# Optimization experiments

Measured on AMD Instinct MI355X. Metric: run time of the kernel, lower is better.

Reference implementation:

```python
import jax, jax.numpy as jnp
import numpy as np

B, S, D, H = 128, 1024, 512, 512


def setup_inputs() -> dict:
    key = jax.random.key(0)
    ks = jax.random.split(key, 8)
    return {
        "input": jax.random.normal(ks[0], (B, D), jnp.float32),
        "context": jax.random.normal(ks[1], (B, S, D), jnp.float32),
        "mask": jax.random.randint(ks[2], (B, S), 0, 2).astype(bool),
        "W_in": jax.random.normal(ks[3], (H, D), jnp.float32) * (1.0 / np.sqrt(D)),
        "b_in": jax.random.normal(ks[4], (H,), jnp.float32) * 0.01,
        "W_ctx": jax.random.normal(ks[5], (H, D), jnp.float32) * (1.0 / np.sqrt(D)),
        "b_ctx": jax.random.normal(ks[6], (H,), jnp.float32) * 0.01,
        "V": jax.random.uniform(ks[7], (H,), jnp.float32, -1.0, 1.0),
    }


def reference(input, context, mask, W_in, b_in, W_ctx, b_ctx, V):
    # inp: [B, H] -> broadcast over S (torch: unsqueeze(2).expand)
    inp = input @ W_in.T + b_in
    # 1x1 Conv1d over permuted context == per-position linear: [B, H, S]
    ctx = jnp.einsum('bsd,hd->bhs', context, W_ctx) + b_ctx[None, :, None]
    # additive (Bahdanau) score: V . tanh(inp + ctx) over H -> [B, S]
    att = jnp.einsum('h,bhs->bs', V, jnp.tanh(inp[:, :, None] + ctx))
    att = jnp.where(mask, -jnp.inf, att)
    alpha = jax.nn.softmax(att, axis=-1)  # [B, S]
    # weighted sum of projected context: [B, H]
    hidden_state = jnp.einsum('bhs,bs->bh', ctx, alpha)
    return (hidden_state, alpha)
```

## Files before the change

### kernel.cpp

```cpp
#include <hip/hip_runtime.h>
#include <math.h>

#define B_ 128
#define S_ 1024
#define D_ 512
#define H_ 512

typedef _Float16 f16x2 __attribute__((ext_vector_type(2)));
typedef _Float16 f16x4 __attribute__((ext_vector_type(4)));
typedef _Float16 f16x8 __attribute__((ext_vector_type(8)));
typedef float    f32x4 __attribute__((ext_vector_type(4)));

__global__ void zero_k(float* __restrict__ p, int n) {
    int i = blockIdx.x * 256 + threadIdx.x;
    if (i < n) p[i] = 0.f;
}

__global__ void init2_k(float* __restrict__ att, float* __restrict__ hidden,
                        const float* __restrict__ bc) {
    int i = blockIdx.x * 256 + threadIdx.x;
    if (i < B_ * S_) att[i] = 0.f;
    else if (i < B_ * S_ + B_ * H_) {
        int j = i - B_ * S_;
        hidden[j] = bc[j & (H_ - 1)];
    }
}

__global__ __launch_bounds__(256) void linear_k(const float* __restrict__ X,
                                                const float* __restrict__ W,
                                                const float* __restrict__ bias,
                                                float* __restrict__ out) {
    int idx = blockIdx.x * 256 + threadIdx.x;
    int b = idx >> 9;
    int h = idx & 511;
    const float4* x = (const float4*)(X + (size_t)b * D_);
    const float4* w = (const float4*)(W + (size_t)h * D_);
    float s = 0.f;
#pragma unroll 8
    for (int k = 0; k < D_ / 4; ++k) {
        float4 xv = x[k], wv = w[k];
        s = fmaf(xv.x, wv.x, s);
        s = fmaf(xv.y, wv.y, s);
        s = fmaf(xv.z, wv.z, s);
        s = fmaf(xv.w, wv.w, s);
    }
    out[idx] = s + bias[h];
}

__device__ inline f16x4 cvt4(float4 v) {
    f16x4 r;
    r[0] = (_Float16)v.x; r[1] = (_Float16)v.y;
    r[2] = (_Float16)v.z; r[3] = (_Float16)v.w;
    return r;
}

__device__ inline float fast_tanh(float x) {
    float e = __expf(2.f * x);
    return 1.f - 2.f / (e + 1.f);
}

template <bool WCTX>
__global__ __launch_bounds__(256) void score_mfma(const float* __restrict__ ctx,
                                                  const float* __restrict__ Wc,
                                                  const float* __restrict__ bc,
                                                  const float* __restrict__ Vv,
                                                  const float* __restrict__ inp,
                                                  float* __restrict__ att,
                                                  _Float16* __restrict__ ctxp) {
    __shared__ __align__(16) _Float16 Ah[128][40];
    __shared__ __align__(16) _Float16 Bh[128][40];
    __shared__ float red[8][128];

    const int tid = threadIdx.x;
    const int s0 = blockIdx.x * 128;
    const int h0 = blockIdx.y * 128;
    const int b  = blockIdx.z;

    const int rb  = tid >> 3;
    const int grp = tid & 7;

    const int wave = tid >> 6;
    const int lane = tid & 63;
    const int wm = wave >> 1, wn = wave & 1;
    const int l15 = lane & 15, quad = lane >> 4;

    const float* Abase = Wc  + (size_t)(h0 + rb) * D_ + grp * 4;
    const float* Bbase = ctx + ((size_t)b * S_ + s0 + rb) * D_ + grp * 4;

    f32x4 acc[4][4];
#pragma unroll
    for (int mi = 0; mi < 4; ++mi)
#pragma unroll
        for (int ni = 0; ni < 4; ++ni) acc[mi][ni] = (f32x4){0.f, 0.f, 0.f, 0.f};

    float4 ra[4], rbv[4];
#pragma unroll
    for (int i = 0; i < 4; ++i) {
        ra[i]  = *(const float4*)(Abase + (size_t)(32 * i) * D_);
        rbv[i] = *(const float4*)(Bbase + (size_t)(32 * i) * D_);
    }

    for (int k0 = 0; k0 < D_; k0 += 32) {
        __syncthreads();
#pragma unroll
        for (int i = 0; i < 4; ++i) {
            const int row = rb + 32 * i;
            *(f16x4*)&Ah[row][grp * 4] = cvt4(ra[i]);
            *(f16x4*)&Bh[row][grp * 4] = cvt4(rbv[i]);
        }
        __syncthreads();
        if (k0 + 32 < D_) {
#pragma unroll
            for (int i = 0; i < 4; ++i) {
                ra[i]  = *(const float4*)(Abase + (size_t)(32 * i) * D_ + k0 + 32);
                rbv[i] = *(const float4*)(Bbase + (size_t)(32 * i) * D_ + k0 + 32);
            }
        }
        f16x8 bhf[4];
#pragma unroll
        for (int ni = 0; ni < 4; ++ni)
            bhf[ni] = *(const f16x8*)&Bh[wn * 64 + ni * 16 + l15][quad * 8];
#pragma unroll
        for (int mi = 0; mi < 4; ++mi) {
            f16x8 ah = *(const f16x8*)&Ah[wm * 64 + mi * 16 + l15][quad * 8];
#pragma unroll
            for (int ni = 0; ni < 4; ++ni)
                acc[mi][ni] = __builtin_amdgcn_mfma_f32_16x16x32_f16(ah, bhf[ni], acc[mi][ni], 0, 0, 0);
        }
    }

    if (WCTX) {
#pragma unroll
        for (int ni = 0; ni < 4; ++ni) {
            const size_t srow = ((size_t)b * S_ + s0 + wn * 64 + ni * 16 + l15) * H_;
#pragma unroll
            for (int mi = 0; mi < 4; ++mi) {
                f16x4 v;
                v[0] = (_Float16)acc[mi][ni][0];
                v[1] = (_Float16)acc[mi][ni][1];
                v[2] = (_Float16)acc[mi][ni][2];
                v[3] = (_Float16)acc[mi][ni][3];
                *(f16x4*)(ctxp + srow + h0 + wm * 64 + mi * 16 + quad * 4) = v;
            }
        }
    }

    float p[4] = {0.f, 0.f, 0.f, 0.f};
#pragma unroll
    for (int mi = 0; mi < 4; ++mi) {
#pragma unroll
        for (int r = 0; r < 4; ++r) {
            const int h = h0 + wm * 64 + mi * 16 + quad * 4 + r;
            const float c  = inp[(size_t)b * H_ + h] + bc[h];
            const float vh = Vv[h];
#pragma unroll
            for (int ni = 0; ni < 4; ++ni)
                p[ni] = fmaf(vh, fast_tanh(c + acc[mi][ni][r]), p[ni]);
        }
    }
    const int cid = wm * 4 + quad;
#pragma unroll
    for (int ni = 0; ni < 4; ++ni)
        red[cid][wn * 64 + ni * 16 + l15] = p[ni];
    __syncthreads();
    if (tid < 128) {
        float s = 0.f;
#pragma unroll
        for (int g = 0; g < 8; ++g) s += red[g][tid];
        atomicAdd(att + (size_t)b * S_ + s0 + tid, s);
    }
}

__global__ __launch_bounds__(256) void softmax_k(const float* __restrict__ att,
                                                 const int* __restrict__ mask,
                                                 float* __restrict__ alpha) {
    const int b = blockIdx.x;
    const int t = threadIdx.x;
    __shared__ float sm[256];
    float v[4];
    float mx = -INFINITY;
#pragma unroll
    for (int i = 0; i < 4; ++i) {
        int s = t + i * 256;
        float a = att[(size_t)b * S_ + s];
        int mk = mask[(size_t)b * S_ + s];
        v[i] = mk ? -INFINITY : a;
        mx = fmaxf(mx, v[i]);
    }
    sm[t] = mx;
    __syncthreads();
    for (int off = 128; off > 0; off >>= 1) {
        if (t < off) sm[t] = fmaxf(sm[t], sm[t + off]);
        __syncthreads();
    }
    mx = sm[0];
    __syncthreads();
    float e[4];
    float sum = 0.f;
#pragma unroll
    for (int i = 0; i < 4; ++i) {
        e[i] = expf(v[i] - mx);
        sum += e[i];
    }
    sm[t] = sum;
    __syncthreads();
    for (int off = 128; off > 0; off >>= 1) {
        if (t < off) sm[t] += sm[t + off];
        __syncthreads();
    }
    float inv = 1.f / sm[0];
#pragma unroll
    for (int i = 0; i < 4; ++i) alpha[(size_t)b * S_ + t + i * 256] = e[i] * inv;
}

__global__ __launch_bounds__(256) void cbar2_k(const _Float16* __restrict__ ctxp,
                                               const float* __restrict__ alpha,
                                               float* __restrict__ hidden) {
    const int b  = blockIdx.y;
    const int s0 = blockIdx.x * 128;
    const int t  = threadIdx.x;
    const int w = t >> 6, lane = t & 63;
    __shared__ float al[128];
    __shared__ float red[3][512];
    if (t < 128) al[t] = alpha[(size_t)b * S_ + s0 + t];
    __syncthreads();
    const _Float16* base = ctxp + ((size_t)b * S_ + s0) * H_ + lane * 8;
    float acc[8] = {0.f, 0.f, 0.f, 0.f, 0.f, 0.f, 0.f, 0.f};
#pragma unroll 4
    for (int s = w; s < 128; s += 4) {
        float a = al[s];
        f16x8 v = *(const f16x8*)(base + (size_t)s * H_);
#pragma unroll
        for (int j = 0; j < 8; ++j) acc[j] = fmaf(a, (float)v[j], acc[j]);
    }
    if (w > 0) {
#pragma unroll
        for (int j = 0; j < 8; ++j) red[w - 1][lane * 8 + j] = acc[j];
    }
    __syncthreads();
    if (w == 0) {
        float* dst = hidden + (size_t)b * H_ + lane * 8;
#pragma unroll
        for (int j = 0; j < 8; ++j)
            atomicAdd(dst + j, acc[j] + red[0][lane * 8 + j] + red[1][lane * 8 + j] + red[2][lane * 8 + j]);
    }
}

__global__ __launch_bounds__(256) void cbar_k(const float* __restrict__ ctx,
                                              const float* __restrict__ alpha,
                                              float* __restrict__ cbar) {
    const int b = blockIdx.y;
    const int s0 = blockIdx.x * 128;
    const int t = threadIdx.x;
    const int c4 = t & 127;
    const int sh = t >> 7;
    __shared__ float al[128];
    __shared__ float4 red[128];
    if (t < 128) al[t] = alpha[(size_t)b * S_ + s0 + t];
    __syncthreads();
    const float4* base = (const float4*)(ctx + ((size_t)b * S_ + s0) * D_);
    float4 c = {0.f, 0.f, 0.f, 0.f};
#pragma unroll 4
    for (int s = sh; s < 128; s += 2) {
        float a = al[s];
        float4 x = base[(size_t)s * (D_ / 4) + c4];
        c.x = fmaf(a, x.x, c.x);
        c.y = fmaf(a, x.y, c.y);
        c.z = fmaf(a, x.z, c.z);
        c.w = fmaf(a, x.w, c.w);
    }
    if (sh == 1) red[c4] = c;
    __syncthreads();
    if (sh == 0) {
        float4 o = red[c4];
        float* dst = cbar + (size_t)b * D_ + c4 * 4;
        atomicAdd(dst + 0, c.x + o.x);
        atomicAdd(dst + 1, c.y + o.y);
        atomicAdd(dst + 2, c.z + o.z);
        atomicAdd(dst + 3, c.w + o.w);
    }
}

extern "C" void kernel_launch(void* const* d_in, const int* in_sizes, int n_in,
                              void* d_out, int out_size, void* d_ws, size_t ws_size,
                              hipStream_t stream) {
    const float* input = (const float*)d_in[0];
    const float* ctx   = (const float*)d_in[1];
    const int*   mask  = (const int*)d_in[2];
    const float* W_in  = (const float*)d_in[3];
    const float* b_in  = (const float*)d_in[4];
    const float* W_ctx = (const float*)d_in[5];
    const float* b_ctx = (const float*)d_in[6];
    const float* V     = (const float*)d_in[7];

    float* hidden = (float*)d_out;
    float* alpha  = (float*)d_out + B_ * H_;

    float* inp  = (float*)d_ws;
    float* att  = inp + B_ * H_;
    float* cbar = att + B_ * S_;
    _Float16* ctxp = (_Float16*)(cbar + B_ * D_);

    const size_t base_bytes = (size_t)(B_ * H_ + B_ * S_ + B_ * D_) * sizeof(float);
    const size_t ctxp_bytes = (size_t)B_ * S_ * H_ * sizeof(_Float16);
    const bool big = ws_size >= base_bytes + ctxp_bytes;

    dim3 g2(S_ / 128, H_ / 128, B_);

    if (big) {
        int ni = B_ * S_ + B_ * H_;
        init2_k<<<(ni + 255) / 256, 256, 0, stream>>>(att, hidden, b_ctx);

        linear_k<<<(B_ * H_) / 256, 256, 0, stream>>>(input, W_in, b_in, inp);

        score_mfma<true><<<g2, 256, 0, stream>>>(ctx, W_ctx, b_ctx, V, inp, att, ctxp);

        softmax_k<<<B_, 256, 0, stream>>>(att, mask, alpha);

        dim3 g4(S_ / 128, B_);
        cbar2_k<<<g4, 256, 0, stream>>>(ctxp, alpha, hidden);
    } else {
        int nz = B_ * S_ + B_ * D_;
        zero_k<<<(nz + 255) / 256, 256, 0, stream>>>(att, nz);

        linear_k<<<(B_ * H_) / 256, 256, 0, stream>>>(input, W_in, b_in, inp);

        score_mfma<false><<<g2, 256, 0, stream>>>(ctx, W_ctx, b_ctx, V, inp, att, nullptr);

        softmax_k<<<B_, 256, 0, stream>>>(att, mask, alpha);

        dim3 g4(S_ / 128, B_);
        cbar_k<<<g4, 256, 0, stream>>>(ctx, alpha, cbar);

        linear_k<<<(B_ * H_) / 256, 256, 0, stream>>>(cbar, W_ctx, b_ctx, hidden);
    }
}
```

Baseline: 567.6 us.

## Double-buffer LDS tiles with XOR swizzle and 16-byte fp16 stores in score GEMM

Replaces the single padded LDS tile and its two barriers per k-step with a ping-pong pair of unpadded buffers, so one barrier per step separates writing the next tile from computing on the current one. Each thread now loads 8 consecutive floats per row and writes a full f16x8 into LDS, at a column offset XOR-swizzled by the row to avoid bank conflicts without padding. The intent is to cut barrier stalls and LDS store instructions and to overlap global loads with MFMA work. In exchange it uses more LDS and adds swizzle index math.

```diff
diff --git a/kernel.cpp b/kernel.cpp
--- a/kernel.cpp
+++ b/kernel.cpp
@@ -6,7 +6,6 @@
 #define D_ 512
 #define H_ 512
 
-typedef _Float16 f16x2 __attribute__((ext_vector_type(2)));
 typedef _Float16 f16x4 __attribute__((ext_vector_type(4)));
 typedef _Float16 f16x8 __attribute__((ext_vector_type(8)));
 typedef float    f32x4 __attribute__((ext_vector_type(4)));
@@ -47,10 +46,12 @@
     out[idx] = s + bias[h];
 }
 
-__device__ inline f16x4 cvt4(float4 v) {
-    f16x4 r;
-    r[0] = (_Float16)v.x; r[1] = (_Float16)v.y;
-    r[2] = (_Float16)v.z; r[3] = (_Float16)v.w;
+__device__ inline f16x8 cvt8(float4 a, float4 b) {
+    f16x8 r;
+    r[0] = (_Float16)a.x; r[1] = (_Float16)a.y;
+    r[2] = (_Float16)a.z; r[3] = (_Float16)a.w;
+    r[4] = (_Float16)b.x; r[5] = (_Float16)b.y;
+    r[6] = (_Float16)b.z; r[7] = (_Float16)b.w;
     return r;
 }
 
@@ -67,8 +68,8 @@
                                                   const float* __restrict__ inp,
                                                   float* __restrict__ att,
                                                   _Float16* __restrict__ ctxp) {
-    __shared__ __align__(16) _Float16 Ah[128][40];
-    __shared__ __align__(16) _Float16 Bh[128][40];
+    __shared__ __align__(16) _Float16 Ah[2][128][32];
+    __shared__ __align__(16) _Float16 Bh[2][128][32];
     __shared__ float red[8][128];
 
     const int tid = threadIdx.x;
@@ -76,16 +77,20 @@
     const int h0 = blockIdx.y * 128;
     const int b  = blockIdx.z;
 
-    const int rb  = tid >> 3;
-    const int grp = tid & 7;
+    const int r0  = tid >> 2;
+    const int kg  = tid & 3;
+    const int swz = ((kg ^ (r0 & 3)) << 3);
 
     const int wave = tid >> 6;
     const int lane = tid & 63;
     const int wm = wave >> 1, wn = wave & 1;
     const int l15 = lane & 15, quad = lane >> 4;
-
-    const float* Abase = Wc  + (size_t)(h0 + rb) * D_ + grp * 4;
-    const float* Bbase = ctx + ((size_t)b * S_ + s0 + rb) * D_ + grp * 4;
+    const int rdsw = ((quad ^ (l15 & 3)) << 3);
+
+    const float* Arow0 = Wc  + (size_t)(h0 + r0) * D_ + kg * 8;
+    const float* Arow1 = Arow0 + (size_t)64 * D_;
+    const float* Brow0 = ctx + ((size_t)b * S_ + s0 + r0) * D_ + kg * 8;
+    const float* Brow1 = Brow0 + (size_t)64 * D_;
 
     f32x4 acc[4][4];
 #pragma unroll
@@ -93,41 +98,52 @@
 #pragma unroll
         for (int ni = 0; ni < 4; ++ni) acc[mi][ni] = (f32x4){0.f, 0.f, 0.f, 0.f};
 
-    float4 ra[4], rbv[4];
-#pragma unroll
-    for (int i = 0; i < 4; ++i) {
-        ra[i]  = *(const float4*)(Abase + (size_t)(32 * i) * D_);
-        rbv[i] = *(const float4*)(Bbase + (size_t)(32 * i) * D_);
-    }
-
-    for (int k0 = 0; k0 < D_; k0 += 32) {
+    float4 A0a, A0b, A1a, A1b, B0a, B0b, B1a, B1b;
+
+#define LOADS(step) do { const int kk_ = (step) * 32;                               \
+    A0a = *(const float4*)(Arow0 + kk_); A0b = *(const float4*)(Arow0 + kk_ + 4);   \
+    A1a = *(const float4*)(Arow1 + kk_); A1b = *(const float4*)(Arow1 + kk_ + 4);   \
+    B0a = *(const float4*)(Brow0 + kk_); B0b = *(const float4*)(Brow0 + kk_ + 4);   \
+    B1a = *(const float4*)(Brow1 + kk_); B1b = *(const float4*)(Brow1 + kk_ + 4); } while (0)
+
+#define WRITE(bf) do {                                                              \
+    *(f16x8*)&Ah[bf][r0][swz]      = cvt8(A0a, A0b);                                \
+    *(f16x8*)&Ah[bf][r0 + 64][swz] = cvt8(A1a, A1b);                                \
+    *(f16x8*)&Bh[bf][r0][swz]      = cvt8(B0a, B0b);                                \
+    *(f16x8*)&Bh[bf][r0 + 64][swz] = cvt8(B1a, B1b); } while (0)
+
+#define COMPUTE(bf) do {                                                            \
+    f16x8 bhf_[4];                                                                  \
+    _Pragma("unroll")                                                               \
+    for (int ni = 0; ni < 4; ++ni)                                                  \
+        bhf_[ni] = *(const f16x8*)&Bh[bf][wn * 64 + ni * 16 + l15][rdsw];           \
+    _Pragma("unroll")                                                               \
+    for (int mi = 0; mi < 4; ++mi) {                                                \
+        f16x8 ah_ = *(const f16x8*)&Ah[bf][wm * 64 + mi * 16 + l15][rdsw];          \
+        _Pragma("unroll")                                                           \
+        for (int ni = 0; ni < 4; ++ni)                                              \
+            acc[mi][ni] = __builtin_amdgcn_mfma_f32_16x16x32_f16(ah_, bhf_[ni],     \
+                                                                 acc[mi][ni], 0, 0, 0); \
+    } } while (0)
+
+    LOADS(0);
+    WRITE(0);
+    LOADS(1);
+    __syncthreads();
+
+    for (int it = 0; it < 16; it += 2) {
+        COMPUTE(0);
+        WRITE(1);
+        if (it + 2 < 16) LOADS(it + 2);
         __syncthreads();
-#pragma unroll
-        for (int i = 0; i < 4; ++i) {
-            const int row = rb + 32 * i;
-            *(f16x4*)&Ah[row][grp * 4] = cvt4(ra[i]);
-            *(f16x4*)&Bh[row][grp * 4] = cvt4(rbv[i]);
-        }
+        COMPUTE(1);
+        if (it + 2 < 16) WRITE(0);
+        if (it + 3 < 16) LOADS(it + 3);
         __syncthreads();
-        if (k0 + 32 < D_) {
-#pragma unroll
-            for (int i = 0; i < 4; ++i) {
-                ra[i]  = *(const float4*)(Abase + (size_t)(32 * i) * D_ + k0 + 32);
-                rbv[i] = *(const float4*)(Bbase + (size_t)(32 * i) * D_ + k0 + 32);
-            }
-        }
-        f16x8 bhf[4];
-#pragma unroll
-        for (int ni = 0; ni < 4; ++ni)
-            bhf[ni] = *(const f16x8*)&Bh[wn * 64 + ni * 16 + l15][quad * 8];
-#pragma unroll
-        for (int mi = 0; mi < 4; ++mi) {
-            f16x8 ah = *(const f16x8*)&Ah[wm * 64 + mi * 16 + l15][quad * 8];
-#pragma unroll
-            for (int ni = 0; ni < 4; ++ni)
-                acc[mi][ni] = __builtin_amdgcn_mfma_f32_16x16x32_f16(ah, bhf[ni], acc[mi][ni], 0, 0, 0);
-        }
-    }
+    }
+#undef LOADS
+#undef WRITE
+#undef COMPUTE
 
     if (WCTX) {
 #pragma unroll
```

Result: faster. 554.0 us (-2.4%).
